# Kernel optimization log

Hardware: AMD Instinct MI355X
Metric: run time of the kernel (lower is better)

Reference implementation:

```python
import jax, jax.numpy as jnp
import numpy as np

B, H, S, D = 4, 16, 2048, 64

def setup_inputs() -> dict:
    key = jax.random.key(0)
    kq, kk, kv = jax.random.split(key, 3)
    Q = jax.random.normal(kq, (B, H, S, D), dtype=jnp.float32)
    K = jax.random.normal(kk, (B, H, S, D), dtype=jnp.float32)
    V = jax.random.normal(kv, (B, H, S, D), dtype=jnp.float32)
    return {"Q": Q, "K": K, "V": V}

def reference(Q, K, V):
    d = Q.shape[-1]
    scale = jnp.sqrt(jnp.asarray(d, dtype=Q.dtype))
    # scores: [B, H, S, S]
    scores = jnp.einsum('bhqd,bhkd->bhqk', Q, K) / scale
    attn = jax.nn.softmax(scores, axis=-1)
    out = jnp.einsum('bhqk,bhkd->bhqd', attn, V)  # [B,H,S,D]
    # permute to [B,S,H,D] then merge heads -> [B,S,H*D]
    b, h, s, dd = out.shape
    return out.transpose(0, 2, 1, 3).reshape(b, s, h * dd)
```

## Files before the change

### kernel.cpp

```cpp
#include <hip/hip_runtime.h>
#include <hip/hip_bf16.h>


#define B_ 4
#define H_ 16
#define S_ 2048
#define D_ 64
#define BH 64
#define NKT 32
#define TILE_USH 4096
#define ARR_USH ((size_t)BH * NKT * TILE_USH)
#define WS_NEED (2 * ARR_USH * 2)
#define QSCALE 0.18033688011112042f

typedef float  f4 __attribute__((ext_vector_type(4)));
typedef short  s4 __attribute__((ext_vector_type(4)));
typedef short  s8 __attribute__((ext_vector_type(8)));
typedef unsigned short ushort_t;

__device__ __forceinline__ unsigned short f2bf(float x) {
  unsigned int u = __float_as_uint(x);
  u += 0x7fffu + ((u >> 16) & 1u);
  return (unsigned short)(u >> 16);
}
__device__ __forceinline__ unsigned int pk_bf16(float a, float b) {
  __hip_bfloat162 h = __float22bfloat162_rn(make_float2(a, b));
  union { __hip_bfloat162 h2; unsigned int u; } cv; cv.h2 = h; return cv.u;
}
__device__ __forceinline__ void splitbf(float x, unsigned short& hi, unsigned short& lo) {
  unsigned int u = __float_as_uint(x);
  hi = (unsigned short)(u >> 16);
  float hf = __uint_as_float(u & 0xffff0000u);
  lo = (unsigned short)(__float_as_uint(x - hf) >> 16);
}

__device__ __forceinline__ f4 mf(s8 a, s8 b, f4 c) {
  return __builtin_amdgcn_mfma_f32_16x16x32_bf16(a, b, c, 0, 0, 0);
}

typedef __attribute__((address_space(1))) const unsigned int* gas_t;
typedef __attribute__((address_space(3))) unsigned int* las_t;
__device__ __forceinline__ void gl_lds16(const void* g, void* l) {
  __builtin_amdgcn_global_load_lds((gas_t)g, (las_t)l, 16, 0, 0);
}

__global__ __launch_bounds__(256)
void prep(const float* __restrict__ K, const float* __restrict__ V,
          ushort_t* __restrict__ KH, ushort_t* __restrict__ VT) {
  __shared__ float Vf[64][68];
  const int tile = blockIdx.x;
  const int t = threadIdx.x;

  const float* vsrc = V + (size_t)tile * 4096;
  float4 vv[4];
  int srow[4], dcol[4];
  #pragma unroll
  for (int r = 0; r < 4; ++r) {
    int f = r * 256 + t; srow[r] = f >> 4; dcol[r] = (f & 15) << 2;
    vv[r] = *(const float4*)(vsrc + srow[r] * 64 + dcol[r]);
  }
  {
    const float* src0 = K + (size_t)tile * 4096;
    #pragma unroll
    for (int u = 0; u < 2; ++u) {
      unsigned int i = u * 256 + t;
      unsigned int row = i >> 3, c = (i & 7) ^ (row & 7);
      const float* src = src0 + row * 64 + c * 8;
      float4 a = *(const float4*)src;
      float4 b = *(const float4*)(src + 4);
      unsigned int d0 = pk_bf16(a.x, a.y), d1 = pk_bf16(a.z, a.w);
      unsigned int d2 = pk_bf16(b.x, b.y), d3 = pk_bf16(b.z, b.w);
      uint4 out = make_uint4(d0, d1, d2, d3);
      *(uint4*)(KH + (size_t)tile * TILE_USH + i * 8) = out;
    }
  }
  #pragma unroll
  for (int r = 0; r < 4; ++r) {
    int pcol = dcol[r] ^ (((srow[r] >> 3) & 3) << 2);
    *(float4*)&Vf[srow[r]][pcol] = vv[r];
  }
  __syncthreads();
  #pragma unroll
  for (int u = 0; u < 2; ++u) {
    unsigned int i = u * 256 + t;
    unsigned int drow = i >> 3, c = (i & 7) ^ (drow & 7);
    const unsigned int ka   = ((c >> 2) << 5) + ((c & 3) << 2);
    const unsigned int colA = drow ^ ((c & 2) << 1);
    const unsigned int colB = colA ^ 8;
    unsigned int d0 = pk_bf16(Vf[ka +  0][colA], Vf[ka +  1][colA]);
    unsigned int d1 = pk_bf16(Vf[ka +  2][colA], Vf[ka +  3][colA]);
    unsigned int d2 = pk_bf16(Vf[ka + 16][colB], Vf[ka + 17][colB]);
    unsigned int d3 = pk_bf16(Vf[ka + 18][colB], Vf[ka + 19][colB]);
    uint4 out = make_uint4(d0, d1, d2, d3);
    *(uint4*)(VT + (size_t)tile * TILE_USH + i * 8) = out;
  }
}

__global__ __launch_bounds__(256, 4)
void attn12(const float* __restrict__ Q, const ushort_t* __restrict__ KH,
            const ushort_t* __restrict__ VT, float* __restrict__ O) {
  __shared__ ushort_t KhS[2][TILE_USH];
  __shared__ ushort_t VtS[2][TILE_USH];

  const int t    = threadIdx.x;
  const int w    = t >> 6;
  const int lane = t & 63;
  const int g    = lane >> 4;
  const int ln   = lane & 15;

  const unsigned int n = blockIdx.x;
  const int bh = (int)((n >> 7) * 8 + (n & 7));
  const int q0 = (int)(((n >> 3) & 15) * 128);

  const size_t tb = (size_t)bh * NKT * TILE_USH;
  const unsigned int cb = w * 128;

  #pragma unroll
  for (int j = 0; j < 2; ++j) {
    const unsigned int ch = cb + 64u * j;
    const size_t go = tb + (size_t)(ch + lane) * 8;
    gl_lds16(KH + go, &KhS[0][ch * 8]);
    gl_lds16(VT + go, &VtS[0][ch * 8]);
  }

  s8 qf[2][2];
  #pragma unroll
  for (int sub = 0; sub < 2; ++sub) {
    const int q = q0 + 32 * w + 16 * sub + ln;
    #pragma unroll
    for (int ks = 0; ks < 2; ++ks) {
      const float* qp = Q + ((size_t)bh * S_ + q) * 64 + 32 * ks + 8 * g;
      float4 a = *(const float4*)qp;
      float4 b = *(const float4*)(qp + 4);
      float xs[8] = {a.x, a.y, a.z, a.w, b.x, b.y, b.z, b.w};
      s8 hv;
      #pragma unroll
      for (int j = 0; j < 8; ++j)
        hv[j] = (short)f2bf(xs[j] * QSCALE);
      qf[sub][ks] = hv;
    }
  }

  f4 oacc[2][4];
  f4 lacc[2];
  #pragma unroll
  for (int s = 0; s < 2; ++s) {
    lacc[s] = (f4)0.0f;
    #pragma unroll
    for (int d = 0; d < 4; ++d) oacc[s][d] = (f4)0.0f;
  }

  s8 ones;
  #pragma unroll
  for (int j = 0; j < 8; ++j) ones[j] = (short)0x3F80;

  unsigned int foff[2];
  #pragma unroll
  for (int ks = 0; ks < 2; ++ks)
    foff[ks] = (unsigned)ln * 128u + (unsigned)(((4 * ks + g) ^ (ln & 7)) * 16);

  for (int kt = 0; kt < NKT; ++kt) {
    const int cur = kt & 1;
    __syncthreads();

    if (kt + 1 < NKT) {
      const size_t tbase = tb + (size_t)(kt + 1) * TILE_USH;
      const int nb = cur ^ 1;
      #pragma unroll
      for (int j = 0; j < 2; ++j) {
        const unsigned int ch = cb + 64u * j;
        const size_t go = tbase + (size_t)(ch + lane) * 8;
        gl_lds16(KH + go, &KhS[nb][ch * 8]);
        gl_lds16(VT + go, &VtS[nb][ch * 8]);
      }
    }

    const char* khb = (const char*)&KhS[cur][0];
    const char* vtb = (const char*)&VtS[cur][0];

    f4 SA[2][2], SB[2][2];
    s8 paA[2], paB[2];

    {
      s8 k0 = *(const s8*)(khb + 0 * 2048 + foff[0]);
      s8 k1 = *(const s8*)(khb + 0 * 2048 + foff[1]);
      s8 k2 = *(const s8*)(khb + 1 * 2048 + foff[0]);
      s8 k3 = *(const s8*)(khb + 1 * 2048 + foff[1]);
      __builtin_amdgcn_s_setprio(1);
      #pragma unroll
      for (int sub = 0; sub < 2; ++sub) {
        f4 x0 = (f4)0.0f, x1 = (f4)0.0f;
        x0 = mf(k0, qf[sub][0], x0); x0 = mf(k1, qf[sub][1], x0);
        x1 = mf(k2, qf[sub][0], x1); x1 = mf(k3, qf[sub][1], x1);
        SA[sub][0] = x0; SA[sub][1] = x1;
      }
      __builtin_amdgcn_s_setprio(0);
    }

    #pragma unroll
    for (int sub = 0; sub < 2; ++sub) {
      f4 x0 = SA[sub][0], x1 = SA[sub][1];
      unsigned int a0 = pk_bf16(__builtin_amdgcn_exp2f(x0[0]),
                                __builtin_amdgcn_exp2f(x0[1]));
      unsigned int a1 = pk_bf16(__builtin_amdgcn_exp2f(x0[2]),
                                __builtin_amdgcn_exp2f(x0[3]));
      unsigned int b0 = pk_bf16(__builtin_amdgcn_exp2f(x1[0]),
                                __builtin_amdgcn_exp2f(x1[1]));
      unsigned int b1 = pk_bf16(__builtin_amdgcn_exp2f(x1[2]),
                                __builtin_amdgcn_exp2f(x1[3]));
      union { unsigned int u[4]; s8 v; } cvp;
      cvp.u[0] = a0; cvp.u[1] = a1; cvp.u[2] = b0; cvp.u[3] = b1;
      paA[sub] = cvp.v;
    }

    {
      s8 k0 = *(const s8*)(khb + 2 * 2048 + foff[0]);
      s8 k1 = *(const s8*)(khb + 2 * 2048 + foff[1]);
      s8 k2 = *(const s8*)(khb + 3 * 2048 + foff[0]);
      s8 k3 = *(const s8*)(khb + 3 * 2048 + foff[1]);
      __builtin_amdgcn_s_setprio(1);
      #pragma unroll
      for (int sub = 0; sub < 2; ++sub) {
        f4 x0 = (f4)0.0f, x1 = (f4)0.0f;
        x0 = mf(k0, qf[sub][0], x0); x0 = mf(k1, qf[sub][1], x0);
        x1 = mf(k2, qf[sub][0], x1); x1 = mf(k3, qf[sub][1], x1);
        SB[sub][0] = x0; SB[sub][1] = x1;
      }
      __builtin_amdgcn_s_setprio(0);
    }

    {
      __builtin_amdgcn_s_setprio(1);
      #pragma unroll
      for (int sub = 0; sub < 2; ++sub)
        lacc[sub] = mf(paA[sub], ones, lacc[sub]);
      #pragma unroll
      for (int dt = 0; dt < 4; ++dt) {
        s8 vb = *(const s8*)(vtb + dt * 2048 + foff[0]);
        #pragma unroll
        for (int sub = 0; sub < 2; ++sub)
          oacc[sub][dt] = mf(paA[sub], vb, oacc[sub][dt]);
      }
      __builtin_amdgcn_s_setprio(0);
    }

    #pragma unroll
    for (int sub = 0; sub < 2; ++sub) {
      f4 x0 = SB[sub][0], x1 = SB[sub][1];
      unsigned int a0 = pk_bf16(__builtin_amdgcn_exp2f(x0[0]),
                                __builtin_amdgcn_exp2f(x0[1]));
      unsigned int a1 = pk_bf16(__builtin_amdgcn_exp2f(x0[2]),
                                __builtin_amdgcn_exp2f(x0[3]));
      unsigned int b0 = pk_bf16(__builtin_amdgcn_exp2f(x1[0]),
                                __builtin_amdgcn_exp2f(x1[1]));
      unsigned int b1 = pk_bf16(__builtin_amdgcn_exp2f(x1[2]),
                                __builtin_amdgcn_exp2f(x1[3]));
      union { unsigned int u[4]; s8 v; } cvp;
      cvp.u[0] = a0; cvp.u[1] = a1; cvp.u[2] = b0; cvp.u[3] = b1;
      paB[sub] = cvp.v;
    }

    {
      __builtin_amdgcn_s_setprio(1);
      #pragma unroll
      for (int sub = 0; sub < 2; ++sub)
        lacc[sub] = mf(paB[sub], ones, lacc[sub]);
      #pragma unroll
      for (int dt = 0; dt < 4; ++dt) {
        s8 vb = *(const s8*)(vtb + dt * 2048 + foff[1]);
        #pragma unroll
        for (int sub = 0; sub < 2; ++sub)
          oacc[sub][dt] = mf(paB[sub], vb, oacc[sub][dt]);
      }
      __builtin_amdgcn_s_setprio(0);
    }
  }

  const int b = bh >> 4, hh = bh & 15;
  #pragma unroll
  for (int sub = 0; sub < 2; ++sub)
    #pragma unroll
    for (int r = 0; r < 4; ++r) {
      const float inv = 1.0f / lacc[sub][r];
      const int q = q0 + 32 * w + 16 * sub + 4 * g + r;
      float* dst = O + ((size_t)b * S_ + q) * (H_ * D_) + hh * 64;
      #pragma unroll
      for (int dt = 0; dt < 4; ++dt)
        dst[16 * dt + ln] = oacc[sub][dt][r] * inv;
    }
}

#define KQ_STR 72
#define VP_STR 76
__global__ __launch_bounds__(256, 2)
void attn_mfma(const float* __restrict__ Q, const float* __restrict__ K,
               const float* __restrict__ V, float* __restrict__ O) {
  __shared__ __align__(16) unsigned short Qh[64][KQ_STR];
  __shared__ __align__(16) unsigned short Ql[64][KQ_STR];
  __shared__ __align__(16) unsigned short Kh[64][KQ_STR];
  __shared__ __align__(16) unsigned short Kl[64][KQ_STR];
  __shared__ __align__(16) unsigned short Vt[64][VP_STR];
  __shared__ __align__(16) unsigned short Pb2[4][16][VP_STR];
  const int t = threadIdx.x, w = t >> 6, lane = t & 63, g = lane >> 4, ln = lane & 15;
  const int bh = blockIdx.x, q0 = blockIdx.y * 64;
  const size_t base = (size_t)bh * S_ * D_;
  {
    const float* Qg = Q + base + (size_t)q0 * D_;
    #pragma unroll
    for (int r = 0; r < 4; ++r) {
      int f = r * 256 + t, row = f >> 4, c4 = (f & 15) << 2;
      float4 v = *(const float4*)(Qg + row * 64 + c4);
      s4 hv, lv; unsigned short hb, lb;
      splitbf(v.x * 0.125f, hb, lb); hv[0] = (short)hb; lv[0] = (short)lb;
      splitbf(v.y * 0.125f, hb, lb); hv[1] = (short)hb; lv[1] = (short)lb;
      splitbf(v.z * 0.125f, hb, lb); hv[2] = (short)hb; lv[2] = (short)lb;
      splitbf(v.w * 0.125f, hb, lb); hv[3] = (short)hb; lv[3] = (short)lb;
      *(s4*)&Qh[row][c4] = hv; *(s4*)&Ql[row][c4] = lv;
    }
  }
  __syncthreads();
  s8 qfh[2], qfl[2];
  #pragma unroll
  for (int ks = 0; ks < 2; ++ks) {
    qfh[ks] = *(const s8*)&Qh[16 * w + ln][ks * 32 + 8 * g];
    qfl[ks] = *(const s8*)&Ql[16 * w + ln][ks * 32 + 8 * g];
  }
  f4 oacc[4]; float m[4], l[4];
  #pragma unroll
  for (int i = 0; i < 4; ++i) { oacc[i] = (f4)0.0f; m[i] = -1e30f; l[i] = 0.0f; }
  const float* Kg = K + base; const float* Vg = V + base;
  float4 kreg[4], vreg[4];
  #pragma unroll
  for (int r = 0; r < 4; ++r) {
    int f = r * 256 + t, row = f >> 4, c4 = (f & 15) << 2;
    kreg[r] = *(const float4*)(Kg + row * 64 + c4);
  }
  #pragma unroll
  for (int j = 0; j < 2; ++j) {
    int it = j * 256 + t, kp = it >> 4, c4 = (it & 15) << 2;
    vreg[2 * j] = *(const float4*)(Vg + (2 * kp) * 64 + c4);
    vreg[2 * j + 1] = *(const float4*)(Vg + (2 * kp + 1) * 64 + c4);
  }
  for (int kt = 0; kt < S_ / 64; ++kt) {
    __syncthreads();
    #pragma unroll
    for (int r = 0; r < 4; ++r) {
      int f = r * 256 + t, row = f >> 4, c4 = (f & 15) << 2;
      float4 v = kreg[r];
      s4 hv, lv; unsigned short hb, lb;
      splitbf(v.x, hb, lb); hv[0] = (short)hb; lv[0] = (short)lb;
      splitbf(v.y, hb, lb); hv[1] = (short)hb; lv[1] = (short)lb;
      splitbf(v.z, hb, lb); hv[2] = (short)hb; lv[2] = (short)lb;
      splitbf(v.w, hb, lb); hv[3] = (short)hb; lv[3] = (short)lb;
      *(s4*)&Kh[row][c4] = hv; *(s4*)&Kl[row][c4] = lv;
    }
    #pragma unroll
    for (int j = 0; j < 2; ++j) {
      int it = j * 256 + t, kp = it >> 4, c4 = (it & 15) << 2;
      float4 a = vreg[2 * j], b = vreg[2 * j + 1];
      float xa[4] = {a.x, a.y, a.z, a.w}, xb[4] = {b.x, b.y, b.z, b.w};
      #pragma unroll
      for (int i = 0; i < 4; ++i) {
        unsigned int pk = (unsigned int)f2bf(xa[i]) | ((unsigned int)f2bf(xb[i]) << 16);
        *(unsigned int*)&Vt[c4 + i][2 * kp] = pk;
      }
    }
    if (kt + 1 < S_ / 64) {
      const float* Kt = Kg + (size_t)(kt + 1) * 4096;
      const float* Vn = Vg + (size_t)(kt + 1) * 4096;
      #pragma unroll
      for (int r = 0; r < 4; ++r) {
        int f = r * 256 + t, row = f >> 4, c4 = (f & 15) << 2;
        kreg[r] = *(const float4*)(Kt + row * 64 + c4);
      }
      #pragma unroll
      for (int j = 0; j < 2; ++j) {
        int it = j * 256 + t, kp = it >> 4, c4 = (it & 15) << 2;
        vreg[2 * j] = *(const float4*)(Vn + (2 * kp) * 64 + c4);
        vreg[2 * j + 1] = *(const float4*)(Vn + (2 * kp + 1) * 64 + c4);
      }
    }
    __syncthreads();
    f4 sacc[4];
    #pragma unroll
    for (int nt = 0; nt < 4; ++nt) sacc[nt] = (f4)0.0f;
    #pragma unroll
    for (int nt = 0; nt < 4; ++nt)
      #pragma unroll
      for (int ks = 0; ks < 2; ++ks) {
        s8 kh = *(const s8*)&Kh[16 * nt + ln][ks * 32 + 8 * g];
        s8 kl = *(const s8*)&Kl[16 * nt + ln][ks * 32 + 8 * g];
        sacc[nt] = __builtin_amdgcn_mfma_f32_16x16x32_bf16(qfh[ks], kh, sacc[nt], 0, 0, 0);
        sacc[nt] = __builtin_amdgcn_mfma_f32_16x16x32_bf16(qfl[ks], kh, sacc[nt], 0, 0, 0);
        sacc[nt] = __builtin_amdgcn_mfma_f32_16x16x32_bf16(qfh[ks], kl, sacc[nt], 0, 0, 0);
      }
    #pragma unroll
    for (int r = 0; r < 4; ++r) {
      float rm = fmaxf(fmaxf(sacc[0][r], sacc[1][r]), fmaxf(sacc[2][r], sacc[3][r]));
      rm = fmaxf(rm, __shfl_xor(rm, 1)); rm = fmaxf(rm, __shfl_xor(rm, 2));
      rm = fmaxf(rm, __shfl_xor(rm, 4)); rm = fmaxf(rm, __shfl_xor(rm, 8));
      float mn = fmaxf(m[r], rm);
      float alpha = __expf(m[r] - mn); m[r] = mn;
      float p0 = __expf(sacc[0][r] - mn), p1 = __expf(sacc[1][r] - mn);
      float p2 = __expf(sacc[2][r] - mn), p3 = __expf(sacc[3][r] - mn);
      float rs = p0 + p1 + p2 + p3;
      rs += __shfl_xor(rs, 1); rs += __shfl_xor(rs, 2);
      rs += __shfl_xor(rs, 4); rs += __shfl_xor(rs, 8);
      l[r] = l[r] * alpha + rs;
      oacc[0][r] *= alpha; oacc[1][r] *= alpha; oacc[2][r] *= alpha; oacc[3][r] *= alpha;
      const int row = 4 * g + r;
      Pb2[w][row][ln] = f2bf(p0); Pb2[w][row][ln + 16] = f2bf(p1);
      Pb2[w][row][ln + 32] = f2bf(p2); Pb2[w][row][ln + 48] = f2bf(p3);
    }
    #pragma unroll
    for (int ks = 0; ks < 2; ++ks) {
      s4 pa0 = *(const s4*)&Pb2[w][ln][ks * 32 + 8 * g];
      s4 pa1 = *(const s4*)&Pb2[w][ln][ks * 32 + 8 * g + 4];
      s8 pa = __builtin_shufflevector(pa0, pa1, 0, 1, 2, 3, 4, 5, 6, 7);
      #pragma unroll
      for (int dt = 0; dt < 4; ++dt) {
        s4 vb0 = *(const s4*)&Vt[16 * dt + ln][ks * 32 + 8 * g];
        s4 vb1 = *(const s4*)&Vt[16 * dt + ln][ks * 32 + 8 * g + 4];
        s8 vb = __builtin_shufflevector(vb0, vb1, 0, 1, 2, 3, 4, 5, 6, 7);
        oacc[dt] = __builtin_amdgcn_mfma_f32_16x16x32_bf16(pa, vb, oacc[dt], 0, 0, 0);
      }
    }
  }
  const int b = bh >> 4, h = bh & 15;
  #pragma unroll
  for (int r = 0; r < 4; ++r) {
    const int q = q0 + 16 * w + 4 * g + r;
    const float inv = 1.0f / l[r];
    float* dst = O + ((size_t)b * S_ + q) * (H_ * D_) + h * 64;
    #pragma unroll
    for (int dt = 0; dt < 4; ++dt) dst[16 * dt + ln] = oacc[dt][r] * inv;
  }
}

extern "C" void kernel_launch(void* const* d_in, const int* in_sizes, int n_in,
                              void* d_out, int out_size, void* d_ws, size_t ws_size,
                              hipStream_t stream) {
  const float* Q = (const float*)d_in[0];
  const float* K = (const float*)d_in[1];
  const float* V = (const float*)d_in[2];
  float* Out = (float*)d_out;
  if (ws_size >= WS_NEED) {
    ushort_t* KHp = (ushort_t*)d_ws;
    ushort_t* VTp = KHp + ARR_USH;
    hipLaunchKernelGGL(prep, dim3(2048), dim3(256), 0, stream, K, V, KHp, VTp);
    hipLaunchKernelGGL(attn12, dim3(1024), dim3(256), 0, stream, Q, KHp, VTp, Out);
  } else {
    hipLaunchKernelGGL(attn_mfma, dim3(BH, S_ / 64), dim3(256), 0, stream, Q, K, V, Out);
  }
}
```

Measured before the change: 199.8 us.

## Halve per-block query tile to 64 rows and double grid size

Each wave now handles one 16-row query sub-tile instead of two, so a block covers 64 queries and the grid doubles to 2048 blocks. Launch bounds rise to 5 blocks per CU, and the block-index mapping is changed to match. Fewer registers per thread and more blocks are meant to improve occupancy and balance across CUs. In exchange, each K/V tile staged in LDS is reused by half as many queries, which doubles global and LDS traffic for K/V.

```diff
diff --git a/kernel.cpp b/kernel.cpp
--- a/kernel.cpp
+++ b/kernel.cpp
@@ -96,8 +96,8 @@
   }
 }
 
-__global__ __launch_bounds__(256, 4)
-void attn12(const float* __restrict__ Q, const ushort_t* __restrict__ KH,
+__global__ __launch_bounds__(256, 5)
+void attn19(const float* __restrict__ Q, const ushort_t* __restrict__ KH,
             const ushort_t* __restrict__ VT, float* __restrict__ O) {
   __shared__ ushort_t KhS[2][TILE_USH];
   __shared__ ushort_t VtS[2][TILE_USH];
@@ -109,8 +109,8 @@
   const int ln   = lane & 15;
 
   const unsigned int n = blockIdx.x;
-  const int bh = (int)((n >> 7) * 8 + (n & 7));
-  const int q0 = (int)(((n >> 3) & 15) * 128);
+  const int bh = (int)((n >> 8) * 8 + (n & 7));
+  const int q0 = (int)(((n >> 3) & 31) * 64);
 
   const size_t tb = (size_t)bh * NKT * TILE_USH;
   const unsigned int cb = w * 128;
@@ -123,10 +123,9 @@
     gl_lds16(VT + go, &VtS[0][ch * 8]);
   }
 
-  s8 qf[2][2];
-  #pragma unroll
-  for (int sub = 0; sub < 2; ++sub) {
-    const int q = q0 + 32 * w + 16 * sub + ln;
+  s8 qf[2];
+  {
+    const int q = q0 + 16 * w + ln;
     #pragma unroll
     for (int ks = 0; ks < 2; ++ks) {
       const float* qp = Q + ((size_t)bh * S_ + q) * 64 + 32 * ks + 8 * g;
@@ -137,18 +136,14 @@
       #pragma unroll
       for (int j = 0; j < 8; ++j)
         hv[j] = (short)f2bf(xs[j] * QSCALE);
-      qf[sub][ks] = hv;
-    }
-  }
-
-  f4 oacc[2][4];
-  f4 lacc[2];
-  #pragma unroll
-  for (int s = 0; s < 2; ++s) {
-    lacc[s] = (f4)0.0f;
-    #pragma unroll
-    for (int d = 0; d < 4; ++d) oacc[s][d] = (f4)0.0f;
-  }
+      qf[ks] = hv;
+    }
+  }
+
+  f4 oacc[4];
+  f4 lacc = (f4)0.0f;
+  #pragma unroll
+  for (int d = 0; d < 4; ++d) oacc[d] = (f4)0.0f;
 
   s8 ones;
   #pragma unroll
@@ -178,8 +173,8 @@
     const char* khb = (const char*)&KhS[cur][0];
     const char* vtb = (const char*)&VtS[cur][0];
 
-    f4 SA[2][2], SB[2][2];
-    s8 paA[2], paB[2];
+    f4 SA0, SA1, SB0, SB1;
+    s8 paA, paB;
 
     {
       s8 k0 = *(const s8*)(khb + 0 * 2048 + foff[0]);
@@ -187,30 +182,25 @@
       s8 k2 = *(const s8*)(khb + 1 * 2048 + foff[0]);
       s8 k3 = *(const s8*)(khb + 1 * 2048 + foff[1]);
       __builtin_amdgcn_s_setprio(1);
-      #pragma unroll
-      for (int sub = 0; sub < 2; ++sub) {
-        f4 x0 = (f4)0.0f, x1 = (f4)0.0f;
-        x0 = mf(k0, qf[sub][0], x0); x0 = mf(k1, qf[sub][1], x0);
-        x1 = mf(k2, qf[sub][0], x1); x1 = mf(k3, qf[sub][1], x1);
-        SA[sub][0] = x0; SA[sub][1] = x1;
-      }
+      f4 x0 = (f4)0.0f, x1 = (f4)0.0f;
+      x0 = mf(k0, qf[0], x0); x0 = mf(k1, qf[1], x0);
+      x1 = mf(k2, qf[0], x1); x1 = mf(k3, qf[1], x1);
+      SA0 = x0; SA1 = x1;
       __builtin_amdgcn_s_setprio(0);
     }
 
-    #pragma unroll
-    for (int sub = 0; sub < 2; ++sub) {
-      f4 x0 = SA[sub][0], x1 = SA[sub][1];
-      unsigned int a0 = pk_bf16(__builtin_amdgcn_exp2f(x0[0]),
-                                __builtin_amdgcn_exp2f(x0[1]));
-      unsigned int a1 = pk_bf16(__builtin_amdgcn_exp2f(x0[2]),
-                                __builtin_amdgcn_exp2f(x0[3]));
-      unsigned int b0 = pk_bf16(__builtin_amdgcn_exp2f(x1[0]),
-                                __builtin_amdgcn_exp2f(x1[1]));
-      unsigned int b1 = pk_bf16(__builtin_amdgcn_exp2f(x1[2]),
-                                __builtin_amdgcn_exp2f(x1[3]));
+    {
+      unsigned int a0 = pk_bf16(__builtin_amdgcn_exp2f(SA0[0]),
+                                __builtin_amdgcn_exp2f(SA0[1]));
+      unsigned int a1 = pk_bf16(__builtin_amdgcn_exp2f(SA0[2]),
+                                __builtin_amdgcn_exp2f(SA0[3]));
+      unsigned int b0 = pk_bf16(__builtin_amdgcn_exp2f(SA1[0]),
+                                __builtin_amdgcn_exp2f(SA1[1]));
+      unsigned int b1 = pk_bf16(__builtin_amdgcn_exp2f(SA1[2]),
+                                __builtin_amdgcn_exp2f(SA1[3]));
       union { unsigned int u[4]; s8 v; } cvp;
       cvp.u[0] = a0; cvp.u[1] = a1; cvp.u[2] = b0; cvp.u[3] = b1;
-      paA[sub] = cvp.v;
+      paA = cvp.v;
     }
 
     {
@@ -219,58 +209,45 @@
       s8 k2 = *(const s8*)(khb + 3 * 2048 + foff[0]);
       s8 k3 = *(const s8*)(khb + 3 * 2048 + foff[1]);
       __builtin_amdgcn_s_setprio(1);
-      #pragma unroll
-      for (int sub = 0; sub < 2; ++sub) {
-        f4 x0 = (f4)0.0f, x1 = (f4)0.0f;
-        x0 = mf(k0, qf[sub][0], x0); x0 = mf(k1, qf[sub][1], x0);
-        x1 = mf(k2, qf[sub][0], x1); x1 = mf(k3, qf[sub][1], x1);
-        SB[sub][0] = x0; SB[sub][1] = x1;
-      }
+      f4 x0 = (f4)0.0f, x1 = (f4)0.0f;
+      x0 = mf(k0, qf[0], x0); x0 = mf(k1, qf[1], x0);
+      x1 = mf(k2, qf[0], x1); x1 = mf(k3, qf[1], x1);
+      SB0 = x0; SB1 = x1;
       __builtin_amdgcn_s_setprio(0);
     }
 
     {
       __builtin_amdgcn_s_setprio(1);
-      #pragma unroll
-      for (int sub = 0; sub < 2; ++sub)
-        lacc[sub] = mf(paA[sub], ones, lacc[sub]);
+      lacc = mf(paA, ones, lacc);
       #pragma unroll
       for (int dt = 0; dt < 4; ++dt) {
         s8 vb = *(const s8*)(vtb + dt * 2048 + foff[0]);
-        #pragma unroll
-        for (int sub = 0; sub < 2; ++sub)
-          oacc[sub][dt] = mf(paA[sub], vb, oacc[sub][dt]);
+        oacc[dt] = mf(paA, vb, oacc[dt]);
       }
       __builtin_amdgcn_s_setprio(0);
     }
 
-    #pragma unroll
-    for (int sub = 0; sub < 2; ++sub) {
-      f4 x0 = SB[sub][0], x1 = SB[sub][1];
-      unsigned int a0 = pk_bf16(__builtin_amdgcn_exp2f(x0[0]),
-                                __builtin_amdgcn_exp2f(x0[1]));
-      unsigned int a1 = pk_bf16(__builtin_amdgcn_exp2f(x0[2]),
-                                __builtin_amdgcn_exp2f(x0[3]));
-      unsigned int b0 = pk_bf16(__builtin_amdgcn_exp2f(x1[0]),
-                                __builtin_amdgcn_exp2f(x1[1]));
-      unsigned int b1 = pk_bf16(__builtin_amdgcn_exp2f(x1[2]),
-                                __builtin_amdgcn_exp2f(x1[3]));
+    {
+      unsigned int a0 = pk_bf16(__builtin_amdgcn_exp2f(SB0[0]),
+                                __builtin_amdgcn_exp2f(SB0[1]));
+      unsigned int a1 = pk_bf16(__builtin_amdgcn_exp2f(SB0[2]),
+                                __builtin_amdgcn_exp2f(SB0[3]));
+      unsigned int b0 = pk_bf16(__builtin_amdgcn_exp2f(SB1[0]),
+                                __builtin_amdgcn_exp2f(SB1[1]));
+      unsigned int b1 = pk_bf16(__builtin_amdgcn_exp2f(SB1[2]),
+                                __builtin_amdgcn_exp2f(SB1[3]));
       union { unsigned int u[4]; s8 v; } cvp;
       cvp.u[0] = a0; cvp.u[1] = a1; cvp.u[2] = b0; cvp.u[3] = b1;
-      paB[sub] = cvp.v;
+      paB = cvp.v;
     }
 
     {
       __builtin_amdgcn_s_setprio(1);
-      #pragma unroll
-      for (int sub = 0; sub < 2; ++sub)
-        lacc[sub] = mf(paB[sub], ones, lacc[sub]);
+      lacc = mf(paB, ones, lacc);
       #pragma unroll
       for (int dt = 0; dt < 4; ++dt) {
         s8 vb = *(const s8*)(vtb + dt * 2048 + foff[1]);
-        #pragma unroll
-        for (int sub = 0; sub < 2; ++sub)
-          oacc[sub][dt] = mf(paB[sub], vb, oacc[sub][dt]);
+        oacc[dt] = mf(paB, vb, oacc[dt]);
       }
       __builtin_amdgcn_s_setprio(0);
     }
@@ -278,16 +255,14 @@
 
   const int b = bh >> 4, hh = bh & 15;
   #pragma unroll
-  for (int sub = 0; sub < 2; ++sub)
-    #pragma unroll
-    for (int r = 0; r < 4; ++r) {
-      const float inv = 1.0f / lacc[sub][r];
-      const int q = q0 + 32 * w + 16 * sub + 4 * g + r;
-      float* dst = O + ((size_t)b * S_ + q) * (H_ * D_) + hh * 64;
-      #pragma unroll
-      for (int dt = 0; dt < 4; ++dt)
-        dst[16 * dt + ln] = oacc[sub][dt][r] * inv;
-    }
+  for (int r = 0; r < 4; ++r) {
+    const float inv = 1.0f / lacc[r];
+    const int q = q0 + 16 * w + 4 * g + r;
+    float* dst = O + ((size_t)b * S_ + q) * (H_ * D_) + hh * 64;
+    #pragma unroll
+    for (int dt = 0; dt < 4; ++dt)
+      dst[16 * dt + ln] = oacc[dt][r] * inv;
+  }
 }
 
 #define KQ_STR 72
@@ -448,7 +423,7 @@
     ushort_t* KHp = (ushort_t*)d_ws;
     ushort_t* VTp = KHp + ARR_USH;
     hipLaunchKernelGGL(prep, dim3(2048), dim3(256), 0, stream, K, V, KHp, VTp);
-    hipLaunchKernelGGL(attn12, dim3(1024), dim3(256), 0, stream, Q, KHp, VTp, Out);
+    hipLaunchKernelGGL(attn19, dim3(2048), dim3(256), 0, stream, Q, KHp, VTp, Out);
   } else {
     hipLaunchKernelGGL(attn_mfma, dim3(BH, S_ / 64), dim3(256), 0, stream, Q, K, V, Out);
   }
```

Result: slower. 207.5 us (+3.8%).
